# Kernel tuning notes

Measured on AMD Instinct MI355X. Metric: run time of the kernel, lower is better.

## Reference

```python
import jax, jax.numpy as jnp
import numpy as np
from math import sqrt

B, S, D, H = 4, 2048, 1024, 16
HD = D // H


def setup_inputs() -> dict:
    key = jax.random.key(0)
    ks = jax.random.split(key, 16)
    w = 0.02
    q = jax.random.normal(ks[0], (B, S, D), jnp.float32)
    k = jax.random.normal(ks[1], (B, S, D), jnp.float32)
    v = jax.random.normal(ks[2], (B, S, D), jnp.float32)
    # causal attention mask [1,1,S,S]
    attn_mask = jnp.tril(jnp.ones((S, S), jnp.int32))[None, None]
    # padding mask [B,1,1,S]; force position 0 valid so no softmax row is all -inf
    pad_mask = jax.random.randint(ks[3], (B, 1, 1, S), 0, 2, jnp.int32)
    pad_mask = pad_mask.at[..., 0].set(1)
    params = {
        'Wq': jax.random.normal(ks[4], (D, D), jnp.float32) * w,
        'bq': jnp.zeros((D,), jnp.float32),
        'Wk': jax.random.normal(ks[5], (D, D), jnp.float32) * w,
        'bk': jnp.zeros((D,), jnp.float32),
        'Wv': jax.random.normal(ks[6], (D, D), jnp.float32) * w,
        'bv': jnp.zeros((D,), jnp.float32),
        'Wo': jax.random.normal(ks[7], (D, D), jnp.float32) * w,
        'bo': jnp.zeros((D,), jnp.float32),
        'gamma': jnp.ones((D,), jnp.float32),
        'beta': jnp.zeros((D,), jnp.float32),
    }
    return dict(q=q, k=k, v=v, attn_mask=attn_mask, pad_mask=pad_mask, **params)


def _mha(q, k, v, Wq, bq, Wk, bk, Wv, bv, Wo, bo, gamma, beta, attn_mask, pad_mask):
    seq = q.shape[1]
    # residual path is detached in the original (q.clone().detach())
    x = jax.lax.stop_gradient(q)
    # Linear projections (torch Linear: y = x @ W.T + b)
    qp = (q @ Wq.T + bq).reshape(-1, H, seq, HD)   # raw view, NO head transpose (faithful)
    kp = (k @ Wk.T + bk).reshape(-1, H, seq, HD)
    vp = (v @ Wv.T + bv).reshape(-1, H, seq, HD)
    scores = jnp.einsum('bhqd,bhkd->bhqk', qp, kp)   # [B,H,S,S]
    scores = jnp.where(pad_mask == 0, -jnp.inf, scores)
    scores = jnp.where(attn_mask == 0, -jnp.inf, scores)
    # scaling applied AFTER masking, as in source
    attn = jax.nn.softmax(scores / sqrt(HD), axis=-1)
    out = jnp.einsum('bhqk,bhkd->bhqd', attn, vp).reshape(-1, seq, D)
    out = out @ Wo.T + bo  # dropout is identity in eval
    y = x + out
    mean = jnp.mean(y, axis=-1, keepdims=True)
    std = jnp.sqrt(jnp.mean((y - mean) ** 2, axis=-1, keepdims=True))
    return gamma * ((y - mean) / (std + 1e-8)) + beta


def reference(q, k, v, attn_mask, pad_mask, Wq, bq, Wk, bk, Wv, bv, Wo, bo, gamma, beta):
    return _mha(q, k, v, Wq, bq, Wk, bk, Wv, bv, Wo, bo, gamma, beta, attn_mask, pad_mask)
```

## Files before the change

kernel.cpp:

```cpp
#include <hip/hip_runtime.h>
#include <hip/hip_bf16.h>
#include <math.h>

#define B_  4
#define S_  2048
#define D_  1024
#define H_  16
#define HD_ 64
#define SD_  (S_*D_)
#define SHD_ (S_*HD_)

typedef __attribute__((ext_vector_type(8))) short          bf16x8;
typedef __attribute__((ext_vector_type(4))) float          f32x4;
typedef __attribute__((ext_vector_type(8))) unsigned short us8;
typedef __attribute__((ext_vector_type(4))) unsigned short us4;

__device__ __forceinline__ unsigned short f2bf(float x) {
  unsigned int u = __float_as_uint(x);
  u += 0x7fffu + ((u >> 16) & 1u);
  return (unsigned short)(u >> 16);
}
__device__ __forceinline__ float bf2f(unsigned short u) {
  return __uint_as_float(((unsigned int)u) << 16);
}

__device__ __forceinline__ void gload16(const unsigned short* g, unsigned short* l) {
  __builtin_amdgcn_global_load_lds(
      (const __attribute__((address_space(1))) unsigned int*)g,
      (__attribute__((address_space(3))) unsigned int*)l,
      16, 0, 0);
}

__device__ __forceinline__ void stage_swz(const unsigned short* __restrict__ g,
                                          int rstride ,
                                          unsigned short* lds, int tid)
{
#pragma unroll
  for (int rr = 0; rr < 2; ++rr) {
    const int cidx = tid + rr * 256;
    const int row  = cidx >> 3;
    const int sb   = ((cidx & 7) * 16) ^ ((row & 7) << 4);
    gload16(g + (size_t)row * rstride + (sb >> 1), lds + cidx * 8);
  }
}

__device__ __forceinline__ void read_frag_pair(const unsigned short* lds, int row,
                                               int quad, bf16x8& f0, bf16x8& f1)
{
  const int sw = (row & 7) << 4;
  const unsigned short* p = lds + row * 64;
  f0 = *(const bf16x8*)(p + (((quad * 16) ^ sw) >> 1));
  f1 = *(const bf16x8*)(p + (((64 + quad * 16) ^ sw) >> 1));
}

__global__ __launch_bounds__(256) void cvt_a(const float* __restrict__ s,
                                             unsigned short* __restrict__ d)
{
  int i = blockIdx.x * 256 + threadIdx.x;
  float4 v = ((const float4*)s)[i];
  us4 o = { f2bf(v.x), f2bf(v.y), f2bf(v.z), f2bf(v.w) };
  *(us4*)(d + (size_t)i * 4) = o;
}

__global__ __launch_bounds__(256) void cvt3(const float* __restrict__ q,
                                            const float* __restrict__ k,
                                            const float* __restrict__ v,
                                            unsigned short* __restrict__ dst)
{
  const float* s = (blockIdx.y == 0) ? q : (blockIdx.y == 1) ? k : v;
  unsigned short* d = dst + (size_t)blockIdx.y * (B_ * (size_t)SD_);
  int i = blockIdx.x * 256 + threadIdx.x;
  float4 x = ((const float4*)s)[i];
  us4 o = { f2bf(x.x), f2bf(x.y), f2bf(x.z), f2bf(x.w) };
  *(us4*)(d + (size_t)i * 4) = o;
}

__global__ __launch_bounds__(256) void cvt_w(const float* __restrict__ w0,
                                             const float* __restrict__ w1,
                                             const float* __restrict__ w2,
                                             const float* __restrict__ w3,
                                             unsigned short* __restrict__ dst)
{
  const float* s = (blockIdx.y == 0) ? w0 : (blockIdx.y == 1) ? w1
                 : (blockIdx.y == 2) ? w2 : w3;
  unsigned short* d = dst + (size_t)blockIdx.y * 1024 * 1024;
  int i = blockIdx.x * 256 + threadIdx.x;
  float4 v = ((const float4*)s)[i];
  us4 o = { f2bf(v.x), f2bf(v.y), f2bf(v.z), f2bf(v.w) };
  *(us4*)(d + (size_t)i * 4) = o;
}

__global__ __launch_bounds__(256) void pad_cvt(const int* __restrict__ pad,
                                               float* __restrict__ padf)
{
  int i = (blockIdx.x * 256 + threadIdx.x) * 4;
  int4 pv = *(const int4*)(pad + i);
  float4 o = { pv.x ? 0.f : -1e30f, pv.y ? 0.f : -1e30f,
               pv.z ? 0.f : -1e30f, pv.w ? 0.f : -1e30f };
  *(float4*)(padf + i) = o;
}

__device__ __forceinline__ void gemm_body(
    const unsigned short* __restrict__ A,
    const unsigned short* __restrict__ Wb,
    const float* __restrict__ bias,
    unsigned short* __restrict__ Cb,
    int n0, int m0)
{
  __shared__ unsigned short As[128 * 32];
  __shared__ unsigned short Bs[128 * 32];

  const int tid  = threadIdx.x;
  const int lane = tid & 63;
  const int w    = tid >> 6;
  const int wm   = w >> 1, wn = w & 1;
  const int l16  = lane & 15, quad = lane >> 4;

  f32x4 acc[4][4];
#pragma unroll
  for (int mt = 0; mt < 4; ++mt)
#pragma unroll
    for (int nt = 0; nt < 4; ++nt) acc[mt][nt] = (f32x4){0.f, 0.f, 0.f, 0.f};

  const int srow = lane >> 2;
  const int sseg = (lane & 3) * 8;

  for (int kt = 0; kt < 32; ++kt) {
    const int kofs = kt * 32;
#pragma unroll
    for (int t = 0; t < 2; ++t) {
      const int r = w * 32 + t * 16 + srow;
      gload16(A  + (size_t)(m0 + r) * 1024 + kofs + sseg, &As[r * 32 + sseg]);
      gload16(Wb + (size_t)(n0 + r) * 1024 + kofs + sseg, &Bs[r * 32 + sseg]);
    }
    __syncthreads();

    bf16x8 af[4], bfr[4];
#pragma unroll
    for (int mt = 0; mt < 4; ++mt)
      af[mt] = *(const bf16x8*)&As[(wm * 64 + mt * 16 + l16) * 32 + quad * 8];
#pragma unroll
    for (int nt = 0; nt < 4; ++nt)
      bfr[nt] = *(const bf16x8*)&Bs[(wn * 64 + nt * 16 + l16) * 32 + quad * 8];
#pragma unroll
    for (int mt = 0; mt < 4; ++mt)
#pragma unroll
      for (int nt = 0; nt < 4; ++nt)
        acc[mt][nt] = __builtin_amdgcn_mfma_f32_16x16x32_bf16(
            af[mt], bfr[nt], acc[mt][nt], 0, 0, 0);
    __syncthreads();
  }

#pragma unroll
  for (int nt = 0; nt < 4; ++nt) {
    const int ncol = n0 + wn * 64 + nt * 16 + l16;
    const float bv = bias[ncol];
#pragma unroll
    for (int mt = 0; mt < 4; ++mt) {
      const int row = m0 + wm * 64 + mt * 16 + quad * 4;
#pragma unroll
      for (int reg = 0; reg < 4; ++reg)
        Cb[(size_t)(row + reg) * 1024 + ncol] = f2bf(acc[mt][nt][reg] + bv);
    }
  }
}

__global__ __launch_bounds__(256) void gemm_mfma(
    const unsigned short* __restrict__ A, const unsigned short* __restrict__ Wb,
    const float* __restrict__ bias, unsigned short* __restrict__ Cb)
{
  gemm_body(A, Wb, bias, Cb, blockIdx.x * 128, blockIdx.y * 128);
}

__global__ __launch_bounds__(256) void gemm_qkv(
    const unsigned short* __restrict__ A3,
    const unsigned short* __restrict__ Wall,
    const float* __restrict__ bq, const float* __restrict__ bk,
    const float* __restrict__ bv,
    unsigned short* __restrict__ Qb, unsigned short* __restrict__ Kb,
    unsigned short* __restrict__ Vb)
{
  const int z = blockIdx.z;
  const unsigned short* A  = A3 + (size_t)z * (B_ * (size_t)SD_);
  const unsigned short* Wb = Wall + (size_t)z * 1024 * 1024;
  const float* bias = (z == 0) ? bq : (z == 1) ? bk : bv;
  unsigned short* Cb = (z == 0) ? Qb : (z == 1) ? Kb : Vb;
  gemm_body(A, Wb, bias, Cb, blockIdx.x * 128, blockIdx.y * 128);
}

__global__ __launch_bounds__(256) void vtrans(
    const unsigned short* __restrict__ V, unsigned short* __restrict__ Vt)
{
  __shared__ unsigned short t[64][72];
  const int tid = threadIdx.x;
  const int st  = blockIdx.x;
  const int bh  = blockIdx.y;
  const unsigned short* src = V + (size_t)bh * SHD_ + (size_t)st * 4096;

#pragma unroll
  for (int u = tid; u < 512; u += 256) {
    us8 vv = ((const us8*)src)[u];
    int s  = u >> 3;
    int dg = (u & 7) * 8;
    *(us8*)&t[s][dg] = vv;
  }
  __syncthreads();

  unsigned short* dst = Vt + (size_t)bh * SHD_ + st * 64;
#pragma unroll
  for (int u = tid; u < 1024; u += 256) {
    int d  = u >> 4;
    int s4 = (u & 15) * 4;
    us4 o = { t[s4][d], t[s4 + 1][d], t[s4 + 2][d], t[s4 + 3][d] };
    *(us4*)(dst + (size_t)d * 2048 + s4) = o;
  }
}

__global__ __launch_bounds__(256, 4) void attn_mfma(
    unsigned short* __restrict__ Qb, const unsigned short* __restrict__ Kb,
    const unsigned short* __restrict__ Vt, const float* __restrict__ padf)
{
  __shared__ unsigned short Ks[64 * 64];
  __shared__ unsigned short Vs[2][64 * 64];
  __shared__ unsigned short Ps[4][16][72];

  const int tid  = threadIdx.x;
  const int lane = tid & 63;
  const int w    = tid >> 6;
  const int p    = blockIdx.x;
  const int bh   = blockIdx.y;
  const int b    = bh >> 4;
  const size_t base = (size_t)bh * SHD_;

  const int l16  = lane & 15;
  const int quad = lane >> 4;

  for (int half = 0; half < 2; ++half) {
    const int it = half ? (31 - p) : p;

    bf16x8 qfrag[2];
    {
      const unsigned short* qrow = Qb + base + (size_t)(it * 64 + w * 16 + l16) * 64;
      qfrag[0] = *(const bf16x8*)(qrow + quad * 8);
      qfrag[1] = *(const bf16x8*)(qrow + 32 + quad * 8);
    }

    f32x4 oacc[4];
#pragma unroll
    for (int dt = 0; dt < 4; ++dt) oacc[dt] = (f32x4){0.f, 0.f, 0.f, 0.f};
    float mS = -INFINITY, lS = 0.f;

    __syncthreads();
    stage_swz(Kb + base, 64, Ks, tid);
    stage_swz(Vt + base, 2048, Vs[0], tid);
    float4 pf[4];
#pragma unroll
    for (int ct = 0; ct < 4; ++ct)
      pf[ct] = *(const float4*)(padf + b * S_ + ct * 16 + quad * 4);
    int cur = 0;

    for (int jt = 0; jt <= it; ++jt) {
      __syncthreads();

      f32x4 sacc[4];
#pragma unroll
      for (int ct = 0; ct < 4; ++ct) {
        bf16x8 k0, k1;
        read_frag_pair(Ks, ct * 16 + l16, quad, k0, k1);
        f32x4 s = (f32x4){0.f, 0.f, 0.f, 0.f};
        s = __builtin_amdgcn_mfma_f32_16x16x32_bf16(k0, qfrag[0], s, 0, 0, 0);
        s = __builtin_amdgcn_mfma_f32_16x16x32_bf16(k1, qfrag[1], s, 0, 0, 0);
        sacc[ct] = s;
      }

      float4 pfn[4];
      if (jt < it) {
        __syncthreads();
        stage_swz(Kb + base + (size_t)(jt + 1) * 4096, 64, Ks, tid);
        stage_swz(Vt + base + (jt + 1) * 64, 2048, Vs[cur ^ 1], tid);
#pragma unroll
        for (int ct = 0; ct < 4; ++ct)
          pfn[ct] = *(const float4*)(padf + b * S_ + (jt + 1) * 64 + ct * 16 + quad * 4);
      }

      float lg[4][4];
      float mx = -INFINITY;
#pragma unroll
      for (int ct = 0; ct < 4; ++ct)
#pragma unroll
        for (int reg = 0; reg < 4; ++reg) {
          float sc = fmaf(sacc[ct][reg], 0.125f, ((const float*)&pf[ct])[reg]);
          if (jt == it) {
            bool ok = (ct * 16 + quad * 4 + reg) <= (w * 16 + l16);
            sc = ok ? sc : -1e30f;
          }
          lg[ct][reg] = sc;
          mx = fmaxf(mx, sc);
        }
      mx = fmaxf(mx, __shfl_xor(mx, 16, 64));
      mx = fmaxf(mx, __shfl_xor(mx, 32, 64));
      const float mnew = fmaxf(mS, mx);
      const float a    = __expf(mS - mnew);
      float sm = 0.f;
#pragma unroll
      for (int ct = 0; ct < 4; ++ct) {
        us4 pk;
#pragma unroll
        for (int reg = 0; reg < 4; ++reg) {
          float pe = __expf(lg[ct][reg] - mnew);
          sm += pe;
          pk[reg] = f2bf(pe);
        }
        *(us4*)&Ps[w][l16][ct * 16 + quad * 4] = pk;
      }
      sm += __shfl_xor(sm, 16, 64);
      sm += __shfl_xor(sm, 32, 64);
      lS = lS * a + sm;
      mS = mnew;

      float aO[4];
#pragma unroll
      for (int reg = 0; reg < 4; ++reg) aO[reg] = __shfl(a, quad * 4 + reg, 64);
#pragma unroll
      for (int dt = 0; dt < 4; ++dt)
#pragma unroll
        for (int reg = 0; reg < 4; ++reg) oacc[dt][reg] *= aO[reg];

      bf16x8 pfrag0 = *(const bf16x8*)&Ps[w][l16][quad * 8];
      bf16x8 pfrag1 = *(const bf16x8*)&Ps[w][l16][32 + quad * 8];
#pragma unroll
      for (int dt = 0; dt < 4; ++dt) {
        bf16x8 v0, v1;
        read_frag_pair(Vs[cur], dt * 16 + l16, quad, v0, v1);
        oacc[dt] = __builtin_amdgcn_mfma_f32_16x16x32_bf16(pfrag0, v0, oacc[dt], 0, 0, 0);
        oacc[dt] = __builtin_amdgcn_mfma_f32_16x16x32_bf16(pfrag1, v1, oacc[dt], 0, 0, 0);
      }

      if (jt < it) {
#pragma unroll
        for (int ct = 0; ct < 4; ++ct) pf[ct] = pfn[ct];
        cur ^= 1;
      }
    }

    float lO[4];
#pragma unroll
    for (int reg = 0; reg < 4; ++reg) lO[reg] = __shfl(lS, quad * 4 + reg, 64);
#pragma unroll
    for (int reg = 0; reg < 4; ++reg) {
      const float rl = 1.0f / lO[reg];
      unsigned short* orow = Qb + base + (size_t)(it * 64 + w * 16 + quad * 4 + reg) * 64;
#pragma unroll
      for (int dt = 0; dt < 4; ++dt)
        orow[dt * 16 + l16] = f2bf(oacc[dt][reg] * rl);
    }
  }
}

__global__ __launch_bounds__(256) void ln_kernel(
    const float* __restrict__ x, const unsigned short* __restrict__ O,
    const float* __restrict__ gamma, const float* __restrict__ beta,
    float* __restrict__ out)
{
  __shared__ float red[8];
  const int row = blockIdx.x;
  const int tid = threadIdx.x;
  float4 xv = ((const float4*)x)[(size_t)row * 256 + tid];
  us4 ov4 = *(const us4*)(O + (size_t)row * 1024 + tid * 4);
  float4 y = make_float4(xv.x + bf2f(ov4[0]), xv.y + bf2f(ov4[1]),
                         xv.z + bf2f(ov4[2]), xv.w + bf2f(ov4[3]));
  float s1 = y.x + y.y + y.z + y.w;
  float s2 = y.x*y.x + y.y*y.y + y.z*y.z + y.w*y.w;
#pragma unroll
  for (int off = 32; off >= 1; off >>= 1) {
    s1 += __shfl_xor(s1, off, 64);
    s2 += __shfl_xor(s2, off, 64);
  }
  if ((tid & 63) == 0) { red[tid >> 6] = s1; red[4 + (tid >> 6)] = s2; }
  __syncthreads();
  s1 = red[0] + red[1] + red[2] + red[3];
  s2 = red[4] + red[5] + red[6] + red[7];
  const float mean = s1 * (1.0f / 1024.0f);
  const float var  = fmaxf(s2 * (1.0f / 1024.0f) - mean * mean, 0.f);
  const float rstd = 1.0f / (sqrtf(var) + 1e-8f);
  float4 gv = ((const float4*)gamma)[tid];
  float4 bv = ((const float4*)beta)[tid];
  float4 r;
  r.x = gv.x * (y.x - mean) * rstd + bv.x;
  r.y = gv.y * (y.y - mean) * rstd + bv.y;
  r.z = gv.z * (y.z - mean) * rstd + bv.z;
  r.w = gv.w * (y.w - mean) * rstd + bv.w;
  ((float4*)out)[(size_t)row * 256 + tid] = r;
}

extern "C" void kernel_launch(void* const* d_in, const int* in_sizes, int n_in,
                              void* d_out, int out_size, void* d_ws, size_t ws_size,
                              hipStream_t stream)
{
  const float* q  = (const float*)d_in[0];
  const float* k  = (const float*)d_in[1];
  const float* v  = (const float*)d_in[2];
  const int*   pad = (const int*)d_in[4];
  const float* Wq = (const float*)d_in[5];
  const float* bq = (const float*)d_in[6];
  const float* Wk = (const float*)d_in[7];
  const float* bk = (const float*)d_in[8];
  const float* Wv = (const float*)d_in[9];
  const float* bv = (const float*)d_in[10];
  const float* Wo = (const float*)d_in[11];
  const float* bo = (const float*)d_in[12];
  const float* gamma = (const float*)d_in[13];
  const float* beta  = (const float*)d_in[14];
  float* out = (float*)d_out;

  char* ws = (char*)d_ws;
  const size_t MB = 1024 * 1024;
  dim3 gg(8, 64), bb(256);

  if (ws_size >= 121 * MB) {
    unsigned short* Ac3  = (unsigned short*)(ws);
    unsigned short* Qb   = (unsigned short*)(ws + 48 * MB);
    unsigned short* Kb   = (unsigned short*)(ws + 64 * MB);
    unsigned short* Vb   = (unsigned short*)(ws + 80 * MB);
    unsigned short* Vtb  = (unsigned short*)(ws + 96 * MB);
    unsigned short* Wall = (unsigned short*)(ws + 112 * MB);
    float*          padf = (float*)(ws + 120 * MB);
    unsigned short* Obuf = Ac3;

    cvt_w<<<dim3(1024, 4), 256, 0, stream>>>(Wq, Wk, Wv, Wo, Wall);
    pad_cvt<<<8, 256, 0, stream>>>(pad, padf);
    cvt3<<<dim3(8192, 3), 256, 0, stream>>>(q, k, v, Ac3);
    gemm_qkv<<<dim3(8, 64, 3), bb, 0, stream>>>(Ac3, Wall, bq, bk, bv, Qb, Kb, Vb);
    vtrans<<<dim3(32, 64), 256, 0, stream>>>(Vb, Vtb);
    attn_mfma<<<dim3(16, 64), 256, 0, stream>>>(Qb, Kb, Vtb, padf);
    gemm_mfma<<<gg, bb, 0, stream>>>(Qb, Wall + 3 * MB, bo, Obuf);
    ln_kernel<<<dim3(B_ * S_), 256, 0, stream>>>(q, Obuf, gamma, beta, out);
  } else {
    unsigned short* Ac   = (unsigned short*)(ws);
    unsigned short* Qb   = (unsigned short*)(ws + 16 * MB);
    unsigned short* Kb   = (unsigned short*)(ws + 32 * MB);
    unsigned short* Vb   = (unsigned short*)(ws + 48 * MB);
    unsigned short* Vtb  = (unsigned short*)(ws + 64 * MB);
    unsigned short* Wall = (unsigned short*)(ws + 80 * MB);
    float*          padf = (float*)(ws + 88 * MB);
    unsigned short* Obuf = Ac;

    cvt_w<<<dim3(1024, 4), 256, 0, stream>>>(Wq, Wk, Wv, Wo, Wall);
    pad_cvt<<<8, 256, 0, stream>>>(pad, padf);
    cvt_a<<<8192, 256, 0, stream>>>(q, Ac);
    gemm_mfma<<<gg, bb, 0, stream>>>(Ac, Wall + 0 * MB, bq, Qb);
    cvt_a<<<8192, 256, 0, stream>>>(k, Ac);
    gemm_mfma<<<gg, bb, 0, stream>>>(Ac, Wall + 1 * MB, bk, Kb);
    cvt_a<<<8192, 256, 0, stream>>>(v, Ac);
    gemm_mfma<<<gg, bb, 0, stream>>>(Ac, Wall + 2 * MB, bv, Vb);
    vtrans<<<dim3(32, 64), 256, 0, stream>>>(Vb, Vtb);
    attn_mfma<<<dim3(16, 64), 256, 0, stream>>>(Qb, Kb, Vtb, padf);
    gemm_mfma<<<gg, bb, 0, stream>>>(Qb, Wall + 3 * MB, bo, Obuf);
    ln_kernel<<<dim3(B_ * S_), 256, 0, stream>>>(q, Obuf, gamma, beta, out);
  }
}
```

Baseline: 388.8 us.

## Double-buffer GEMM LDS staging, swizzle blocks across XCDs, fuse conversion kernels

The GEMM main loop now uses two LDS buffers, prefetching the next K tile with async global-to-LDS loads while MFMAs run on the current one, and synchronizes with explicit vmcnt waits and raw barriers. Block indices are remapped so consecutive tiles land on the same XCD to improve L2 reuse. The three separate q/k/v, weight and pad conversion launches are merged into one kernel to cut launch overhead. LDS use doubles, and the hand-written waitcnt logic relies on exact knowledge of how many loads are in flight.

```diff
diff --git a/kernel.cpp b/kernel.cpp
--- a/kernel.cpp
+++ b/kernel.cpp
@@ -62,19 +62,6 @@
   *(us4*)(d + (size_t)i * 4) = o;
 }
 
-__global__ __launch_bounds__(256) void cvt3(const float* __restrict__ q,
-                                            const float* __restrict__ k,
-                                            const float* __restrict__ v,
-                                            unsigned short* __restrict__ dst)
-{
-  const float* s = (blockIdx.y == 0) ? q : (blockIdx.y == 1) ? k : v;
-  unsigned short* d = dst + (size_t)blockIdx.y * (B_ * (size_t)SD_);
-  int i = blockIdx.x * 256 + threadIdx.x;
-  float4 x = ((const float4*)s)[i];
-  us4 o = { f2bf(x.x), f2bf(x.y), f2bf(x.z), f2bf(x.w) };
-  *(us4*)(d + (size_t)i * 4) = o;
-}
-
 __global__ __launch_bounds__(256) void cvt_w(const float* __restrict__ w0,
                                              const float* __restrict__ w1,
                                              const float* __restrict__ w2,
@@ -100,6 +87,42 @@
   *(float4*)(padf + i) = o;
 }
 
+__global__ __launch_bounds__(256) void cvt_all(
+    const float* __restrict__ q, const float* __restrict__ k,
+    const float* __restrict__ v,
+    const float* __restrict__ w0, const float* __restrict__ w1,
+    const float* __restrict__ w2, const float* __restrict__ w3,
+    const int* __restrict__ pad,
+    unsigned short* __restrict__ Ac3, unsigned short* __restrict__ Wall,
+    float* __restrict__ padf)
+{
+  const int bx = blockIdx.x;
+  if (bx < 24576) {
+    const int y = bx >> 13;
+    const int i = (bx & 8191) * 256 + threadIdx.x;
+    const float* s = (y == 0) ? q : (y == 1) ? k : v;
+    unsigned short* d = Ac3 + (size_t)y * (B_ * (size_t)SD_);
+    float4 x = ((const float4*)s)[i];
+    us4 o = { f2bf(x.x), f2bf(x.y), f2bf(x.z), f2bf(x.w) };
+    *(us4*)(d + (size_t)i * 4) = o;
+  } else if (bx < 24576 + 4096) {
+    const int bw = bx - 24576;
+    const int y = bw >> 10;
+    const int i = (bw & 1023) * 256 + threadIdx.x;
+    const float* s = (y == 0) ? w0 : (y == 1) ? w1 : (y == 2) ? w2 : w3;
+    unsigned short* d = Wall + (size_t)y * 1024 * 1024;
+    float4 x = ((const float4*)s)[i];
+    us4 o = { f2bf(x.x), f2bf(x.y), f2bf(x.z), f2bf(x.w) };
+    *(us4*)(d + (size_t)i * 4) = o;
+  } else {
+    const int i = ((bx - 28672) * 256 + threadIdx.x) * 4;
+    int4 pv = *(const int4*)(pad + i);
+    float4 o = { pv.x ? 0.f : -1e30f, pv.y ? 0.f : -1e30f,
+                 pv.z ? 0.f : -1e30f, pv.w ? 0.f : -1e30f };
+    *(float4*)(padf + i) = o;
+  }
+}
+
 __device__ __forceinline__ void gemm_body(
     const unsigned short* __restrict__ A,
     const unsigned short* __restrict__ Wb,
@@ -107,8 +130,8 @@
     unsigned short* __restrict__ Cb,
     int n0, int m0)
 {
-  __shared__ unsigned short As[128 * 32];
-  __shared__ unsigned short Bs[128 * 32];
+  __shared__ unsigned short As[2][128 * 32];
+  __shared__ unsigned short Bs[2][128 * 32];
 
   const int tid  = threadIdx.x;
   const int lane = tid & 63;
@@ -124,31 +147,50 @@
 
   const int srow = lane >> 2;
   const int sseg = (lane & 3) * 8;
-
+  const int r0   = w * 32 + srow;
+
+  const unsigned short* Ar0 = A  + (size_t)(m0 + r0) * 1024 + sseg;
+  const unsigned short* Ar1 = A  + (size_t)(m0 + r0 + 16) * 1024 + sseg;
+  const unsigned short* Br0 = Wb + (size_t)(n0 + r0) * 1024 + sseg;
+  const unsigned short* Br1 = Wb + (size_t)(n0 + r0 + 16) * 1024 + sseg;
+
+  auto STAGE = [&](int buf, int kt) {
+    const int ko = kt * 32;
+    gload16(Ar0 + ko, &As[buf][r0 * 32 + sseg]);
+    gload16(Ar1 + ko, &As[buf][(r0 + 16) * 32 + sseg]);
+    gload16(Br0 + ko, &Bs[buf][r0 * 32 + sseg]);
+    gload16(Br1 + ko, &Bs[buf][(r0 + 16) * 32 + sseg]);
+  };
+
+  STAGE(0, 0);
+  int cur = 0;
   for (int kt = 0; kt < 32; ++kt) {
-    const int kofs = kt * 32;
-#pragma unroll
-    for (int t = 0; t < 2; ++t) {
-      const int r = w * 32 + t * 16 + srow;
-      gload16(A  + (size_t)(m0 + r) * 1024 + kofs + sseg, &As[r * 32 + sseg]);
-      gload16(Wb + (size_t)(n0 + r) * 1024 + kofs + sseg, &Bs[r * 32 + sseg]);
+    if (kt < 31) {
+      STAGE(cur ^ 1, kt + 1);
+      asm volatile("s_waitcnt vmcnt(4)" ::: "memory");
+    } else {
+      asm volatile("s_waitcnt vmcnt(0)" ::: "memory");
     }
-    __syncthreads();
+    __builtin_amdgcn_sched_barrier(0);
+    __builtin_amdgcn_s_barrier();
 
     bf16x8 af[4], bfr[4];
 #pragma unroll
     for (int mt = 0; mt < 4; ++mt)
-      af[mt] = *(const bf16x8*)&As[(wm * 64 + mt * 16 + l16) * 32 + quad * 8];
+      af[mt] = *(const bf16x8*)&As[cur][(wm * 64 + mt * 16 + l16) * 32 + quad * 8];
 #pragma unroll
     for (int nt = 0; nt < 4; ++nt)
-      bfr[nt] = *(const bf16x8*)&Bs[(wn * 64 + nt * 16 + l16) * 32 + quad * 8];
+      bfr[nt] = *(const bf16x8*)&Bs[cur][(wn * 64 + nt * 16 + l16) * 32 + quad * 8];
 #pragma unroll
     for (int mt = 0; mt < 4; ++mt)
 #pragma unroll
       for (int nt = 0; nt < 4; ++nt)
         acc[mt][nt] = __builtin_amdgcn_mfma_f32_16x16x32_bf16(
             af[mt], bfr[nt], acc[mt][nt], 0, 0, 0);
-    __syncthreads();
+
+    __builtin_amdgcn_sched_barrier(0);
+    __builtin_amdgcn_s_barrier();
+    cur ^= 1;
   }
 
 #pragma unroll
@@ -165,11 +207,23 @@
   }
 }
 
+__device__ __forceinline__ void xcd_coords(int& n0, int& m0)
+{
+  const int nwgx = gridDim.x;
+  const int nwg  = nwgx * gridDim.y;
+  const int bid  = blockIdx.y * nwgx + blockIdx.x;
+  const int sw   = (bid & 7) * (nwg >> 3) + (bid >> 3);
+  n0 = (sw % nwgx) * 128;
+  m0 = (sw / nwgx) * 128;
+}
+
 __global__ __launch_bounds__(256) void gemm_mfma(
     const unsigned short* __restrict__ A, const unsigned short* __restrict__ Wb,
     const float* __restrict__ bias, unsigned short* __restrict__ Cb)
 {
-  gemm_body(A, Wb, bias, Cb, blockIdx.x * 128, blockIdx.y * 128);
+  int n0, m0;
+  xcd_coords(n0, m0);
+  gemm_body(A, Wb, bias, Cb, n0, m0);
 }
 
 __global__ __launch_bounds__(256) void gemm_qkv(
@@ -185,7 +239,9 @@
   const unsigned short* Wb = Wall + (size_t)z * 1024 * 1024;
   const float* bias = (z == 0) ? bq : (z == 1) ? bk : bv;
   unsigned short* Cb = (z == 0) ? Qb : (z == 1) ? Kb : Vb;
-  gemm_body(A, Wb, bias, Cb, blockIdx.x * 128, blockIdx.y * 128);
+  int n0, m0;
+  xcd_coords(n0, m0);
+  gemm_body(A, Wb, bias, Cb, n0, m0);
 }
 
 __global__ __launch_bounds__(256) void vtrans(
@@ -427,9 +483,8 @@
     float*          padf = (float*)(ws + 120 * MB);
     unsigned short* Obuf = Ac3;
 
-    cvt_w<<<dim3(1024, 4), 256, 0, stream>>>(Wq, Wk, Wv, Wo, Wall);
-    pad_cvt<<<8, 256, 0, stream>>>(pad, padf);
-    cvt3<<<dim3(8192, 3), 256, 0, stream>>>(q, k, v, Ac3);
+    cvt_all<<<dim3(28680), 256, 0, stream>>>(q, k, v, Wq, Wk, Wv, Wo, pad,
+                                             Ac3, Wall, padf);
     gemm_qkv<<<dim3(8, 64, 3), bb, 0, stream>>>(Ac3, Wall, bq, bk, bv, Qb, Kb, Vb);
     vtrans<<<dim3(32, 64), 256, 0, stream>>>(Vb, Vtb);
     attn_mfma<<<dim3(16, 64), 256, 0, stream>>>(Qb, Kb, Vtb, padf);
```

Result: no change. 381.4 us (-1.9%).
